# Optimization experiments

Measured on AMD Instinct MI355X. Metric: run time of the kernel, lower is better.

Reference implementation:

```python
import jax, jax.numpy as jnp
import numpy as np

B, C, H, W = 16, 256, 64, 64

def setup_inputs() -> dict:
    key = jax.random.key(0)
    ks = jax.random.split(key, 4)
    scale = 1.0 / np.sqrt(C)
    return {
        "x": jax.random.normal(ks[0], (B, C, H, W), dtype=jnp.float32),
        "w1": jax.random.normal(ks[1], (C, C), dtype=jnp.float32) * scale,
        "b1": jnp.zeros((C,), dtype=jnp.float32),
        "w2": jax.random.normal(ks[2], (C, C), dtype=jnp.float32) * scale,
        "b2": jnp.zeros((C,), dtype=jnp.float32),
        "w3": jax.random.normal(ks[3], (C, C), dtype=jnp.float32) * scale,
        "b3": jnp.zeros((C,), dtype=jnp.float32),
    }

def reference(x, w1, b1, w2, b2, w3, b3):
    b, c, h, w = x.shape
    n = h * w
    # 1x1 convs == per-pixel linear maps over channels; w has shape [C_out, C_in]
    def proj(wt, bias):
        return jnp.einsum('bchw,oc->bohw', x, wt) + bias[None, :, None, None]
    v = proj(w1, b1).reshape(b, c, n).transpose(0, 2, 1)   # [B, N, C]
    q = proj(w2, b2).reshape(b, c, n)                      # [B, C, N]
    k = proj(w3, b3).reshape(b, c, n)                      # [B, C, N]
    weight = jnp.einsum('bcn,bdn->bcd', q, k)              # [B, C, C]
    # global softmax over the entire flattened C*C matrix per batch element
    weight = jax.nn.softmax(weight.reshape(b, -1), axis=1).reshape(b, c, c)
    out = jnp.einsum('bnc,bcd->bdn', v, weight)            # [B, C, N]
    return out.reshape(x.shape)
```

## Files before the change

### kernel.cpp

```cpp
#include <hip/hip_runtime.h>


typedef unsigned short u16;
typedef __attribute__((ext_vector_type(8))) short short8;
typedef __attribute__((ext_vector_type(4))) float floatx4;

__device__ __forceinline__ u16 f2b(float f) {
  union { float f; unsigned int u; } v; v.f = f;
  unsigned int u = v.u;
  return (u16)((u + 0x7fffu + ((u >> 16) & 1u)) >> 16);
}
__device__ __forceinline__ float b2f(u16 h) {
  union { unsigned int u; float f; } v; v.u = ((unsigned int)h) << 16;
  return v.f;
}

__global__ __launch_bounds__(256) void prep_w_kernel(
    const float* __restrict__ w1, const float* __restrict__ w2, const float* __restrict__ w3,
    u16* __restrict__ W1Th, u16* __restrict__ W2h, u16* __restrict__ W2l,
    u16* __restrict__ W3h, u16* __restrict__ W3l, float* __restrict__ xsum) {
  const int blk = blockIdx.x, t = threadIdx.x;
  if (blk == 576) {
#pragma unroll
    for (int i = 0; i < 16; ++i) xsum[t + i * 256] = 0.f;
    return;
  }
  if (blk < 64) {
    __shared__ float tile[32][33];
    const int e0 = (blk & 7) * 32, c0 = (blk >> 3) * 32;
    const int tx = t & 31, ty = t >> 5;
#pragma unroll
    for (int i = 0; i < 4; ++i)
      tile[ty + i * 8][tx] = w1[(c0 + ty + i * 8) * 256 + e0 + tx];
    __syncthreads();
#pragma unroll
    for (int i = 0; i < 4; ++i)
      W1Th[(e0 + ty + i * 8) * 256 + c0 + tx] = f2b(tile[tx][ty + i * 8]);
  } else {
    const int i = (blk - 64) * 256 + t;
    const int e = i & 0xffff;
    const float f = (i >> 16) ? w3[e] : w2[e];
    u16 h = f2b(f);
    if (i >> 16) { W3h[e] = h; W3l[e] = f2b(f - b2f(h)); }
    else         { W2h[e] = h; W2l[e] = f2b(f - b2f(h)); }
  }
}

__device__ __forceinline__ void stage8(const float4 a, const float4 b,
                                       u16* dH, u16* dL, float& xa) {
  const float f[8] = {a.x, a.y, a.z, a.w, b.x, b.y, b.z, b.w};
  union { u16 h8[8]; uint4 q; } uh, ul;
#pragma unroll
  for (int i = 0; i < 8; ++i) {
    const u16 hi = f2b(f[i]);
    uh.h8[i] = hi;
    ul.h8[i] = f2b(f[i] - b2f(hi));
    xa += f[i];
  }
  *(uint4*)dH = uh.q;
  *(uint4*)dL = ul.q;
}

__global__ __launch_bounds__(512, 2) void gram_kernel(
    const float* __restrict__ x, float* __restrict__ Gp, float* __restrict__ xsum) {
  constexpr int LR = 40;
  __shared__ u16 lH[2][256 * LR], lL[2][256 * LR];
  const int b = blockIdx.x >> 4, s = (blockIdx.x >> 1) & 7, mh = blockIdx.x & 1;
  const float* Xb = x + (long)b * 1048576 + s * 512;
  const int t = threadIdx.x;
  const int lane = t & 63, wave = t >> 6;
  const int quad = lane >> 4, l16 = lane & 15;
  const int wml = (wave & 1) * 64 + mh * 128;
  const int wn = (wave >> 1) * 64;
  const int r0 = t >> 2, qc = (t & 3) * 8;
  const int r1 = r0 + 128;
  floatx4 acc[4][4] = {};
  float xa0 = 0.f, xa1 = 0.f;
  float4 p[4];
  p[0] = *(const float4*)(Xb + (long)r0 * 4096 + qc);
  p[1] = *(const float4*)(Xb + (long)r0 * 4096 + qc + 4);
  p[2] = *(const float4*)(Xb + (long)r1 * 4096 + qc);
  p[3] = *(const float4*)(Xb + (long)r1 * 4096 + qc + 4);
  stage8(p[0], p[1], lH[0] + r0 * LR + qc, lL[0] + r0 * LR + qc, xa0);
  stage8(p[2], p[3], lH[0] + r1 * LR + qc, lL[0] + r1 * LR + qc, xa1);
  __syncthreads();
  for (int kb = 0; kb < 16; ++kb) {
    const int cur = kb & 1, nxt = cur ^ 1;
    if (kb < 15) {
      const long kk = (kb + 1) * 32;
      p[0] = *(const float4*)(Xb + (long)r0 * 4096 + kk + qc);
      p[1] = *(const float4*)(Xb + (long)r0 * 4096 + kk + qc + 4);
      p[2] = *(const float4*)(Xb + (long)r1 * 4096 + kk + qc);
      p[3] = *(const float4*)(Xb + (long)r1 * 4096 + kk + qc + 4);
    }
    const u16* cH = lH[cur];
    const u16* cL = lL[cur];
    short8 ah[4], al[4];
#pragma unroll
    for (int i = 0; i < 4; ++i) {
      ah[i] = *(const short8*)(cH + (wml + i * 16 + l16) * LR + quad * 8);
      al[i] = *(const short8*)(cL + (wml + i * 16 + l16) * LR + quad * 8);
    }
#pragma unroll
    for (int j = 0; j < 4; ++j) {
      const short8 bh = *(const short8*)(cH + (wn + j * 16 + l16) * LR + quad * 8);
      const short8 bl = *(const short8*)(cL + (wn + j * 16 + l16) * LR + quad * 8);
#pragma unroll
      for (int i = 0; i < 4; ++i) {
        acc[i][j] = __builtin_amdgcn_mfma_f32_16x16x32_bf16(ah[i], bh, acc[i][j], 0, 0, 0);
        acc[i][j] = __builtin_amdgcn_mfma_f32_16x16x32_bf16(ah[i], bl, acc[i][j], 0, 0, 0);
        acc[i][j] = __builtin_amdgcn_mfma_f32_16x16x32_bf16(al[i], bh, acc[i][j], 0, 0, 0);
      }
    }
    if (kb < 15) {
      stage8(p[0], p[1], lH[nxt] + r0 * LR + qc, lL[nxt] + r0 * LR + qc, xa0);
      stage8(p[2], p[3], lH[nxt] + r1 * LR + qc, lL[nxt] + r1 * LR + qc, xa1);
    }
    __syncthreads();
  }
  if (mh == 0) {
    float v = xa0;
    v += __shfl_xor(v, 1);
    v += __shfl_xor(v, 2);
    if ((t & 3) == 0) atomicAdd(&xsum[b * 256 + r0], v);
    v = xa1;
    v += __shfl_xor(v, 1);
    v += __shfl_xor(v, 2);
    if ((t & 3) == 0) atomicAdd(&xsum[b * 256 + r1], v);
  }
  float* G = Gp + ((long)b * 8 + s) * 65536;
#pragma unroll
  for (int i = 0; i < 4; ++i) {
    const int row0 = wml + i * 16 + quad * 4;
#pragma unroll
    for (int j = 0; j < 4; ++j) {
      const int col = wn + j * 16 + l16;
#pragma unroll
      for (int r = 0; r < 4; ++r)
        G[(long)(row0 + r) * 256 + col] = acc[i][j][r];
    }
  }
}

__global__ void reduce_g_kernel(const float* __restrict__ Gp, u16* __restrict__ Gh,
                                u16* __restrict__ Gl) {
  const long e = (long)blockIdx.x * 256 + threadIdx.x;
  const long base = ((e >> 16) << 19) + (e & 65535);
  float s = 0.f;
#pragma unroll
  for (int i = 0; i < 8; ++i) s += Gp[base + (long)i * 65536];
  u16 h = f2b(s);
  Gh[e] = h;
  Gl[e] = f2b(s - b2f(h));
}

template <bool X3, int EPI>
__global__ __launch_bounds__(256) void gemm_small(
    const u16* __restrict__ Ah, const u16* __restrict__ Al,
    const u16* __restrict__ Bh, const u16* __restrict__ Bl,
    long aBatch, long bBatch, long oBatch,
    float* __restrict__ outF, u16* __restrict__ outH, u16* __restrict__ outL) {
  constexpr int LR = 40;
  __shared__ u16 smem[(X3 ? 4 : 2) * 64 * LR];
  u16* lAh = smem;
  u16* lBh = smem + 64 * LR;
  u16* lAl = X3 ? (smem + 2 * 64 * LR) : nullptr;
  u16* lBl = X3 ? (smem + 3 * 64 * LR) : nullptr;
  const int b = blockIdx.z;
  const int tm = blockIdx.x & 3, tn = blockIdx.x >> 2;
  const u16* Ahb = Ah + (long)b * aBatch + (long)tm * 64 * 256;
  const u16* Bhb = Bh + (long)b * bBatch + (long)tn * 64 * 256;
  const u16* Alb = X3 ? (Al + (long)b * aBatch + (long)tm * 64 * 256) : nullptr;
  const u16* Blb = X3 ? (Bl + (long)b * bBatch + (long)tn * 64 * 256) : nullptr;
  const int t = threadIdx.x;
  const int lane = t & 63, wave = t >> 6;
  const int quad = lane >> 4, l16 = lane & 15;
  const int wm = (wave & 1) * 32, wn = (wave >> 1) * 32;
  const int r = t >> 2, qc = (t & 3) * 8;
  floatx4 acc[2][2] = {};
  for (int kk = 0; kk < 256; kk += 32) {
    __syncthreads();
    *(uint4*)(lAh + r * LR + qc) = *(const uint4*)(Ahb + (long)r * 256 + kk + qc);
    *(uint4*)(lBh + r * LR + qc) = *(const uint4*)(Bhb + (long)r * 256 + kk + qc);
    if (X3) {
      *(uint4*)(lAl + r * LR + qc) = *(const uint4*)(Alb + (long)r * 256 + kk + qc);
      *(uint4*)(lBl + r * LR + qc) = *(const uint4*)(Blb + (long)r * 256 + kk + qc);
    }
    __syncthreads();
    short8 afh[2], bfh[2], afl[2], bfl[2];
#pragma unroll
    for (int i = 0; i < 2; ++i) {
      afh[i] = *(const short8*)(lAh + (wm + i * 16 + l16) * LR + quad * 8);
      bfh[i] = *(const short8*)(lBh + (wn + i * 16 + l16) * LR + quad * 8);
      if (X3) {
        afl[i] = *(const short8*)(lAl + (wm + i * 16 + l16) * LR + quad * 8);
        bfl[i] = *(const short8*)(lBl + (wn + i * 16 + l16) * LR + quad * 8);
      }
    }
#pragma unroll
    for (int i = 0; i < 2; ++i)
#pragma unroll
      for (int j = 0; j < 2; ++j) {
        acc[i][j] = __builtin_amdgcn_mfma_f32_16x16x32_bf16(afh[i], bfh[j], acc[i][j], 0, 0, 0);
        if (X3) {
          acc[i][j] = __builtin_amdgcn_mfma_f32_16x16x32_bf16(afh[i], bfl[j], acc[i][j], 0, 0, 0);
          acc[i][j] = __builtin_amdgcn_mfma_f32_16x16x32_bf16(afl[i], bfh[j], acc[i][j], 0, 0, 0);
        }
      }
  }
  const long obase = (long)b * oBatch;
#pragma unroll
  for (int i = 0; i < 2; ++i) {
    const int mb = tm * 64 + wm + i * 16 + quad * 4;
#pragma unroll
    for (int j = 0; j < 2; ++j) {
      const int n = tn * 64 + wn + j * 16 + l16;
#pragma unroll
      for (int rr = 0; rr < 4; ++rr) {
        const float v = acc[i][j][rr];
        const long idx = obase + (long)(mb + rr) * 256 + n;
        if (EPI == 0) {
          outF[idx] = v;
        } else if (EPI == 1) {
          u16 h = f2b(v);
          outH[idx] = h;
          outL[idx] = f2b(v - b2f(h));
        } else {
          outH[idx] = f2b(v);
        }
      }
    }
  }
}

__global__ __launch_bounds__(256, 2) void gemm_out(
    const u16* __restrict__ Mh, const float* __restrict__ x,
    const float* __restrict__ bb, float* __restrict__ out) {
  constexpr int LR = 40;
  __shared__ u16 lA[256 * LR], lB[128 * LR];
  const int b = blockIdx.z;
  const int tn = blockIdx.x;
  const u16* Ab = Mh + (long)b * 65536;
  const float* Xb = x + (long)b * 1048576 + tn * 128;
  const int t = threadIdx.x;
  const int lane = t & 63, wave = t >> 6;
  const int quad = lane >> 4, l16 = lane & 15;
  const int wm = wave * 64;
  const int erp = (t >> 4) * 2;
  const int n0 = (t & 15) * 8;
  floatx4 acc[4][8] = {};
  for (int kk = 0; kk < 256; kk += 32) {
    __syncthreads();
#pragma unroll
    for (int h = 0; h < 4; ++h) {
      const int r = (t >> 2) + h * 64;
      *(uint4*)(lA + r * LR + (t & 3) * 8) =
          *(const uint4*)(Ab + (long)r * 256 + kk + (t & 3) * 8);
    }
    {
      const float4 a0 = *(const float4*)(Xb + (long)(kk + erp) * 4096 + n0);
      const float4 a1 = *(const float4*)(Xb + (long)(kk + erp) * 4096 + n0 + 4);
      const float4 c0 = *(const float4*)(Xb + (long)(kk + erp + 1) * 4096 + n0);
      const float4 c1 = *(const float4*)(Xb + (long)(kk + erp + 1) * 4096 + n0 + 4);
      const float fa[8] = {a0.x, a0.y, a0.z, a0.w, a1.x, a1.y, a1.z, a1.w};
      const float fc[8] = {c0.x, c0.y, c0.z, c0.w, c1.x, c1.y, c1.z, c1.w};
#pragma unroll
      for (int i = 0; i < 8; ++i) {
        const int nl = n0 + i;
        const int sb = (erp >> 3) ^ ((nl >> 4) & 3);
        const unsigned int pk =
            (unsigned int)f2b(fa[i]) | ((unsigned int)f2b(fc[i]) << 16);
        *(unsigned int*)(lB + nl * LR + sb * 8 + (erp & 7)) = pk;
      }
    }
    __syncthreads();
    short8 af[4], bf[8];
#pragma unroll
    for (int j = 0; j < 8; ++j) {
      const int n = j * 16 + l16;
      const int rb = quad ^ ((n >> 4) & 3);
      bf[j] = *(const short8*)(lB + n * LR + rb * 8);
    }
#pragma unroll
    for (int i = 0; i < 4; ++i)
      af[i] = *(const short8*)(lA + (wm + i * 16 + l16) * LR + quad * 8);
#pragma unroll
    for (int i = 0; i < 4; ++i)
#pragma unroll
      for (int j = 0; j < 8; ++j)
        acc[i][j] = __builtin_amdgcn_mfma_f32_16x16x32_bf16(af[i], bf[j], acc[i][j], 0, 0, 0);
  }
  const long obase = (long)b * 1048576;
#pragma unroll
  for (int i = 0; i < 4; ++i) {
    const int mb = wm + i * 16 + quad * 4;
#pragma unroll
    for (int j = 0; j < 8; ++j) {
      const int n = tn * 128 + j * 16 + l16;
#pragma unroll
      for (int r = 0; r < 4; ++r)
        out[obase + (long)(mb + r) * 4096 + n] = acc[i][j][r] + bb[b * 256 + mb + r];
    }
  }
}

__global__ __launch_bounds__(512) void bias_prep_kernel(
    const float* __restrict__ w2, const float* __restrict__ w3,
    const float* __restrict__ xsum, float* __restrict__ S2, float* __restrict__ S3) {
  __shared__ float xs[256];
  const int b = blockIdx.x, t = threadIdx.x;
  if (t < 256) xs[t] = xsum[b * 256 + t];
  __syncthreads();
  const float* wm = (t < 256) ? w2 : w3;
  const int a = t & 255;
  float s = 0.f;
#pragma unroll 4
  for (int c = 0; c < 256; ++c) s += wm[a * 256 + c] * xs[c];
  if (t < 256) S2[b * 256 + a] = s;
  else         S3[b * 256 + a] = s;
}

__global__ __launch_bounds__(256) void softmax_pass1(
    const float* __restrict__ Lt, const float* __restrict__ S2, const float* __restrict__ S3,
    const float* __restrict__ b2, const float* __restrict__ b3,
    float* __restrict__ bm, float* __restrict__ bs) {
  __shared__ float ls2[256], lb2[256];
  __shared__ float redm[4], reds[4];
  const int b = blockIdx.y, blk = blockIdx.x, t = threadIdx.x;
  ls2[t] = S2[b * 256 + t];
  lb2[t] = b2[t];
  __syncthreads();
  const int fw0 = blk * 2048 + t * 8;
  const int d = fw0 >> 8, a0 = fw0 & 255;
  const float c1 = b3[d];
  const float c0 = S3[b * 256 + d] + 4096.f * c1;
  const long base = (long)b * 65536 + fw0;
  float4 v0 = *(const float4*)(Lt + base);
  float4 v1 = *(const float4*)(Lt + base + 4);
  float v[8] = {v0.x, v0.y, v0.z, v0.w, v1.x, v1.y, v1.z, v1.w};
  float m = -3.4e38f;
#pragma unroll
  for (int i = 0; i < 8; ++i) {
    v[i] += lb2[a0 + i] * c0 + c1 * ls2[a0 + i];
    m = fmaxf(m, v[i]);
  }
  for (int o = 32; o; o >>= 1) m = fmaxf(m, __shfl_xor(m, o));
  const int wid = t >> 6, lane = t & 63;
  if (lane == 0) redm[wid] = m;
  __syncthreads();
  const float bmax = fmaxf(fmaxf(redm[0], redm[1]), fmaxf(redm[2], redm[3]));
  float s = 0.f;
#pragma unroll
  for (int i = 0; i < 8; ++i) s += __expf(v[i] - bmax);
  for (int o = 32; o; o >>= 1) s += __shfl_xor(s, o);
  if (lane == 0) reds[wid] = s;
  __syncthreads();
  if (t == 0) {
    bm[b * 32 + blk] = bmax;
    bs[b * 32 + blk] = reds[0] + reds[1] + reds[2] + reds[3];
  }
}

__global__ __launch_bounds__(256) void softmax_pass3(
    const float* __restrict__ Lt, const float* __restrict__ S2, const float* __restrict__ S3,
    const float* __restrict__ b2, const float* __restrict__ b3,
    const float* __restrict__ bm, const float* __restrict__ bs,
    const float* __restrict__ b1, u16* __restrict__ WTh, float* __restrict__ bb) {
  __shared__ float ls2[256], lb2[256], lb1[256];
  __shared__ float sM, sInv;
  const int b = blockIdx.y, blk = blockIdx.x, t = threadIdx.x;
  if (t < 64) {
    const float m = (t < 32) ? bm[b * 32 + t] : -3.4e38f;
    float s = (t < 32) ? bs[b * 32 + t] : 0.f;
    float M = m;
    for (int o = 32; o; o >>= 1) M = fmaxf(M, __shfl_xor(M, o));
    s *= __expf(m - M);
    for (int o = 32; o; o >>= 1) s += __shfl_xor(s, o);
    if (t == 0) { sM = M; sInv = 1.0f / s; }
  }
  ls2[t] = S2[b * 256 + t];
  lb2[t] = b2[t];
  lb1[t] = b1[t];
  __syncthreads();
  const float M = sM, inv = sInv;
  const int fw0 = blk * 2048 + t * 8;
  const int d = fw0 >> 8, a0 = fw0 & 255;
  const float c1 = b3[d];
  const float c0 = S3[b * 256 + d] + 4096.f * c1;
  const long base = (long)b * 65536 + fw0;
  float4 v0 = *(const float4*)(Lt + base);
  float4 v1 = *(const float4*)(Lt + base + 4);
  float v[8] = {v0.x, v0.y, v0.z, v0.w, v1.x, v1.y, v1.z, v1.w};
  union { u16 h[8]; uint4 q; } o;
  float bsum = 0.f;
#pragma unroll
  for (int i = 0; i < 8; ++i) {
    const float vv = v[i] + lb2[a0 + i] * c0 + c1 * ls2[a0 + i];
    const float w = __expf(vv - M) * inv;
    o.h[i] = f2b(w);
    bsum += w * lb1[a0 + i];
  }
  *(uint4*)(WTh + base) = o.q;
  for (int off = 16; off; off >>= 1) bsum += __shfl_xor(bsum, off);
  if ((t & 31) == 0) bb[b * 256 + d] = bsum;
}

extern "C" void kernel_launch(void* const* d_in, const int* in_sizes, int n_in,
                              void* d_out, int out_size, void* d_ws, size_t ws_size,
                              hipStream_t stream) {
  const float* x  = (const float*)d_in[0];
  const float* w1 = (const float*)d_in[1];
  const float* b1 = (const float*)d_in[2];
  const float* w2 = (const float*)d_in[3];
  const float* b2 = (const float*)d_in[4];
  const float* w3 = (const float*)d_in[5];
  const float* b3 = (const float*)d_in[6];
  float* out = (float*)d_out;

  char* ws = (char*)d_ws;
  size_t off = 0;
  auto alloc = [&](size_t bytes) {
    void* p = ws + off;
    off += (bytes + 255) & ~(size_t)255;
    return p;
  };
  float* Gp = (float*)alloc(8ull * 16 * 65536 * 4);
  float* xsum = (float*)alloc(16 * 256 * 4);
  u16* Gh   = (u16*)alloc(16ull * 65536 * 2);
  u16* Gl   = (u16*)alloc(16ull * 65536 * 2);
  u16* T3h  = (u16*)alloc(16ull * 65536 * 2);
  u16* T3l  = (u16*)alloc(16ull * 65536 * 2);
  float* Lb = (float*)alloc(16ull * 65536 * 4);
  u16* WTh  = (u16*)alloc(16ull * 65536 * 2);
  u16* Mh   = (u16*)alloc(16ull * 65536 * 2);
  u16* W1Th = (u16*)alloc(65536 * 2);
  u16* W2h  = (u16*)alloc(65536 * 2);
  u16* W2l  = (u16*)alloc(65536 * 2);
  u16* W3h  = (u16*)alloc(65536 * 2);
  u16* W3l  = (u16*)alloc(65536 * 2);
  float* S2   = (float*)alloc(16 * 256 * 4);
  float* S3   = (float*)alloc(16 * 256 * 4);
  float* bmx  = (float*)alloc(16 * 32 * 4);
  float* bsx  = (float*)alloc(16 * 32 * 4);
  float* bb   = (float*)alloc(16 * 256 * 4);

  prep_w_kernel<<<577, 256, 0, stream>>>(w1, w2, w3, W1Th, W2h, W2l, W3h, W3l, xsum);

  gram_kernel<<<256, 512, 0, stream>>>(x, Gp, xsum);
  reduce_g_kernel<<<4096, 256, 0, stream>>>(Gp, Gh, Gl);

  gemm_small<true, 1><<<dim3(16, 1, 16), 256, 0, stream>>>(
      W3h, W3l, Gh, Gl, 0, 65536, 65536, nullptr, T3h, T3l);
  gemm_small<true, 0><<<dim3(16, 1, 16), 256, 0, stream>>>(
      T3h, T3l, W2h, W2l, 65536, 0, 65536, Lb, nullptr, nullptr);

  bias_prep_kernel<<<16, 512, 0, stream>>>(w2, w3, xsum, S2, S3);
  softmax_pass1<<<dim3(32, 16), 256, 0, stream>>>(Lb, S2, S3, b2, b3, bmx, bsx);
  softmax_pass3<<<dim3(32, 16), 256, 0, stream>>>(Lb, S2, S3, b2, b3, bmx, bsx,
                                                  b1, WTh, bb);

  gemm_small<false, 2><<<dim3(16, 1, 16), 256, 0, stream>>>(
      WTh, nullptr, W1Th, nullptr, 65536, 0, 65536, nullptr, Mh, nullptr);
  gemm_out<<<dim3(32, 1, 16), 256, 0, stream>>>(Mh, x, bb, out);
}
```

Measured before the change: 217.4 us.

## Split gram over more K-slices, swizzle LDS, packed bf16 cvt, register-prefetch GEMMs

The gram kernel now splits the pixel dimension into 16 slices instead of 8, doubling the grid to 512 blocks. Its LDS tiles drop the padding in favour of an XOR swizzle, and the launch bound asks for 4 blocks per CU. Float-to-bf16 conversion uses the packed v_cvt_pk_bf16_f32 instruction in place of manual rounding. gemm_small and gemm_out gain register prefetch of the next K tile so global loads overlap the MFMA work. In exchange, the partial Gram buffer doubles, which means more write traffic and a heavier reduce_g pass.

```diff
diff --git a/kernel.cpp b/kernel.cpp
--- a/kernel.cpp
+++ b/kernel.cpp
@@ -13,6 +13,11 @@
 __device__ __forceinline__ float b2f(u16 h) {
   union { unsigned int u; float f; } v; v.u = ((unsigned int)h) << 16;
   return v.f;
+}
+__device__ __forceinline__ unsigned int cvt_pk_bf16(float lo, float hi) {
+  unsigned int r;
+  asm("v_cvt_pk_bf16_f32 %0, %1, %2" : "=v"(r) : "v"(lo), "v"(hi));
+  return r;
 }
 
 __global__ __launch_bounds__(256) void prep_w_kernel(
@@ -49,24 +54,26 @@
 __device__ __forceinline__ void stage8(const float4 a, const float4 b,
                                        u16* dH, u16* dL, float& xa) {
   const float f[8] = {a.x, a.y, a.z, a.w, b.x, b.y, b.z, b.w};
-  union { u16 h8[8]; uint4 q; } uh, ul;
-#pragma unroll
-  for (int i = 0; i < 8; ++i) {
-    const u16 hi = f2b(f[i]);
-    uh.h8[i] = hi;
-    ul.h8[i] = f2b(f[i] - b2f(hi));
-    xa += f[i];
+  union { unsigned int w[4]; uint4 q; } uh, ul;
+#pragma unroll
+  for (int i = 0; i < 4; ++i) {
+    const unsigned int h = cvt_pk_bf16(f[2 * i], f[2 * i + 1]);
+    uh.w[i] = h;
+    union { unsigned int u; float ff; } h0, h1;
+    h0.u = h << 16;
+    h1.u = h & 0xffff0000u;
+    ul.w[i] = cvt_pk_bf16(f[2 * i] - h0.ff, f[2 * i + 1] - h1.ff);
+    xa += f[2 * i] + f[2 * i + 1];
   }
   *(uint4*)dH = uh.q;
   *(uint4*)dL = ul.q;
 }
 
-__global__ __launch_bounds__(512, 2) void gram_kernel(
+__global__ __launch_bounds__(512, 4) void gram_kernel(
     const float* __restrict__ x, float* __restrict__ Gp, float* __restrict__ xsum) {
-  constexpr int LR = 40;
-  __shared__ u16 lH[2][256 * LR], lL[2][256 * LR];
-  const int b = blockIdx.x >> 4, s = (blockIdx.x >> 1) & 7, mh = blockIdx.x & 1;
-  const float* Xb = x + (long)b * 1048576 + s * 512;
+  __shared__ u16 lH[2][256 * 32], lL[2][256 * 32];
+  const int b = blockIdx.x >> 5, s = (blockIdx.x >> 1) & 15, mh = blockIdx.x & 1;
+  const float* Xb = x + (long)b * 1048576 + s * 256;
   const int t = threadIdx.x;
   const int lane = t & 63, wave = t >> 6;
   const int quad = lane >> 4, l16 = lane & 15;
@@ -74,6 +81,8 @@
   const int wn = (wave >> 1) * 64;
   const int r0 = t >> 2, qc = (t & 3) * 8;
   const int r1 = r0 + 128;
+  const int wq = (((t & 3) ^ ((r0 >> 1) & 3))) * 8;
+  const int rq = ((quad ^ ((l16 >> 1) & 3))) * 8;
   floatx4 acc[4][4] = {};
   float xa0 = 0.f, xa1 = 0.f;
   float4 p[4];
@@ -81,12 +90,12 @@
   p[1] = *(const float4*)(Xb + (long)r0 * 4096 + qc + 4);
   p[2] = *(const float4*)(Xb + (long)r1 * 4096 + qc);
   p[3] = *(const float4*)(Xb + (long)r1 * 4096 + qc + 4);
-  stage8(p[0], p[1], lH[0] + r0 * LR + qc, lL[0] + r0 * LR + qc, xa0);
-  stage8(p[2], p[3], lH[0] + r1 * LR + qc, lL[0] + r1 * LR + qc, xa1);
+  stage8(p[0], p[1], lH[0] + r0 * 32 + wq, lL[0] + r0 * 32 + wq, xa0);
+  stage8(p[2], p[3], lH[0] + r1 * 32 + wq, lL[0] + r1 * 32 + wq, xa1);
   __syncthreads();
-  for (int kb = 0; kb < 16; ++kb) {
+  for (int kb = 0; kb < 8; ++kb) {
     const int cur = kb & 1, nxt = cur ^ 1;
-    if (kb < 15) {
+    if (kb < 7) {
       const long kk = (kb + 1) * 32;
       p[0] = *(const float4*)(Xb + (long)r0 * 4096 + kk + qc);
       p[1] = *(const float4*)(Xb + (long)r0 * 4096 + kk + qc + 4);
@@ -98,13 +107,13 @@
     short8 ah[4], al[4];
 #pragma unroll
     for (int i = 0; i < 4; ++i) {
-      ah[i] = *(const short8*)(cH + (wml + i * 16 + l16) * LR + quad * 8);
-      al[i] = *(const short8*)(cL + (wml + i * 16 + l16) * LR + quad * 8);
+      ah[i] = *(const short8*)(cH + (wml + i * 16 + l16) * 32 + rq);
+      al[i] = *(const short8*)(cL + (wml + i * 16 + l16) * 32 + rq);
     }
 #pragma unroll
     for (int j = 0; j < 4; ++j) {
-      const short8 bh = *(const short8*)(cH + (wn + j * 16 + l16) * LR + quad * 8);
-      const short8 bl = *(const short8*)(cL + (wn + j * 16 + l16) * LR + quad * 8);
+      const short8 bh = *(const short8*)(cH + (wn + j * 16 + l16) * 32 + rq);
+      const short8 bl = *(const short8*)(cL + (wn + j * 16 + l16) * 32 + rq);
 #pragma unroll
       for (int i = 0; i < 4; ++i) {
         acc[i][j] = __builtin_amdgcn_mfma_f32_16x16x32_bf16(ah[i], bh, acc[i][j], 0, 0, 0);
@@ -112,9 +121,9 @@
         acc[i][j] = __builtin_amdgcn_mfma_f32_16x16x32_bf16(al[i], bh, acc[i][j], 0, 0, 0);
       }
     }
-    if (kb < 15) {
-      stage8(p[0], p[1], lH[nxt] + r0 * LR + qc, lL[nxt] + r0 * LR + qc, xa0);
-      stage8(p[2], p[3], lH[nxt] + r1 * LR + qc, lL[nxt] + r1 * LR + qc, xa1);
+    if (kb < 7) {
+      stage8(p[0], p[1], lH[nxt] + r0 * 32 + wq, lL[nxt] + r0 * 32 + wq, xa0);
+      stage8(p[2], p[3], lH[nxt] + r1 * 32 + wq, lL[nxt] + r1 * 32 + wq, xa1);
     }
     __syncthreads();
   }
@@ -128,7 +137,7 @@
     v += __shfl_xor(v, 2);
     if ((t & 3) == 0) atomicAdd(&xsum[b * 256 + r1], v);
   }
-  float* G = Gp + ((long)b * 8 + s) * 65536;
+  float* G = Gp + ((long)b * 16 + s) * 65536;
 #pragma unroll
   for (int i = 0; i < 4; ++i) {
     const int row0 = wml + i * 16 + quad * 4;
@@ -145,10 +154,10 @@
 __global__ void reduce_g_kernel(const float* __restrict__ Gp, u16* __restrict__ Gh,
                                 u16* __restrict__ Gl) {
   const long e = (long)blockIdx.x * 256 + threadIdx.x;
-  const long base = ((e >> 16) << 19) + (e & 65535);
+  const long base = ((e >> 16) << 20) + (e & 65535);
   float s = 0.f;
 #pragma unroll
-  for (int i = 0; i < 8; ++i) s += Gp[base + (long)i * 65536];
+  for (int i = 0; i < 16; ++i) s += Gp[base + (long)i * 65536];
   u16 h = f2b(s);
   Gh[e] = h;
   Gl[e] = f2b(s - b2f(h));
@@ -178,15 +187,30 @@
   const int wm = (wave & 1) * 32, wn = (wave >> 1) * 32;
   const int r = t >> 2, qc = (t & 3) * 8;
   floatx4 acc[2][2] = {};
+  uint4 pA, pB, pAl = {}, pBl = {};
+  pA = *(const uint4*)(Ahb + (long)r * 256 + qc);
+  pB = *(const uint4*)(Bhb + (long)r * 256 + qc);
+  if (X3) {
+    pAl = *(const uint4*)(Alb + (long)r * 256 + qc);
+    pBl = *(const uint4*)(Blb + (long)r * 256 + qc);
+  }
   for (int kk = 0; kk < 256; kk += 32) {
     __syncthreads();
-    *(uint4*)(lAh + r * LR + qc) = *(const uint4*)(Ahb + (long)r * 256 + kk + qc);
-    *(uint4*)(lBh + r * LR + qc) = *(const uint4*)(Bhb + (long)r * 256 + kk + qc);
+    *(uint4*)(lAh + r * LR + qc) = pA;
+    *(uint4*)(lBh + r * LR + qc) = pB;
     if (X3) {
-      *(uint4*)(lAl + r * LR + qc) = *(const uint4*)(Alb + (long)r * 256 + kk + qc);
-      *(uint4*)(lBl + r * LR + qc) = *(const uint4*)(Blb + (long)r * 256 + kk + qc);
+      *(uint4*)(lAl + r * LR + qc) = pAl;
+      *(uint4*)(lBl + r * LR + qc) = pBl;
     }
     __syncthreads();
+    if (kk < 224) {
+      pA = *(const uint4*)(Ahb + (long)r * 256 + kk + 32 + qc);
+      pB = *(const uint4*)(Bhb + (long)r * 256 + kk + 32 + qc);
+      if (X3) {
+        pAl = *(const uint4*)(Alb + (long)r * 256 + kk + 32 + qc);
+        pBl = *(const uint4*)(Blb + (long)r * 256 + kk + 32 + qc);
+      }
+    }
     short8 afh[2], bfh[2], afl[2], bfl[2];
 #pragma unroll
     for (int i = 0; i < 2; ++i) {
@@ -249,31 +273,44 @@
   const int erp = (t >> 4) * 2;
   const int n0 = (t & 15) * 8;
   floatx4 acc[4][8] = {};
+  uint4 pA[4];
+  float4 pb0, pb1, pb2, pb3;
+#pragma unroll
+  for (int h = 0; h < 4; ++h)
+    pA[h] = *(const uint4*)(Ab + (long)((t >> 2) + h * 64) * 256 + (t & 3) * 8);
+  pb0 = *(const float4*)(Xb + (long)erp * 4096 + n0);
+  pb1 = *(const float4*)(Xb + (long)erp * 4096 + n0 + 4);
+  pb2 = *(const float4*)(Xb + (long)(erp + 1) * 4096 + n0);
+  pb3 = *(const float4*)(Xb + (long)(erp + 1) * 4096 + n0 + 4);
   for (int kk = 0; kk < 256; kk += 32) {
     __syncthreads();
 #pragma unroll
     for (int h = 0; h < 4; ++h) {
       const int r = (t >> 2) + h * 64;
-      *(uint4*)(lA + r * LR + (t & 3) * 8) =
-          *(const uint4*)(Ab + (long)r * 256 + kk + (t & 3) * 8);
+      *(uint4*)(lA + r * LR + (t & 3) * 8) = pA[h];
     }
     {
-      const float4 a0 = *(const float4*)(Xb + (long)(kk + erp) * 4096 + n0);
-      const float4 a1 = *(const float4*)(Xb + (long)(kk + erp) * 4096 + n0 + 4);
-      const float4 c0 = *(const float4*)(Xb + (long)(kk + erp + 1) * 4096 + n0);
-      const float4 c1 = *(const float4*)(Xb + (long)(kk + erp + 1) * 4096 + n0 + 4);
-      const float fa[8] = {a0.x, a0.y, a0.z, a0.w, a1.x, a1.y, a1.z, a1.w};
-      const float fc[8] = {c0.x, c0.y, c0.z, c0.w, c1.x, c1.y, c1.z, c1.w};
+      const float fa[8] = {pb0.x, pb0.y, pb0.z, pb0.w, pb1.x, pb1.y, pb1.z, pb1.w};
+      const float fc[8] = {pb2.x, pb2.y, pb2.z, pb2.w, pb3.x, pb3.y, pb3.z, pb3.w};
 #pragma unroll
       for (int i = 0; i < 8; ++i) {
         const int nl = n0 + i;
         const int sb = (erp >> 3) ^ ((nl >> 4) & 3);
-        const unsigned int pk =
-            (unsigned int)f2b(fa[i]) | ((unsigned int)f2b(fc[i]) << 16);
-        *(unsigned int*)(lB + nl * LR + sb * 8 + (erp & 7)) = pk;
+        *(unsigned int*)(lB + nl * LR + sb * 8 + (erp & 7)) =
+            cvt_pk_bf16(fa[i], fc[i]);
       }
     }
     __syncthreads();
+    if (kk < 224) {
+      const int k2 = kk + 32;
+#pragma unroll
+      for (int h = 0; h < 4; ++h)
+        pA[h] = *(const uint4*)(Ab + (long)((t >> 2) + h * 64) * 256 + k2 + (t & 3) * 8);
+      pb0 = *(const float4*)(Xb + (long)(k2 + erp) * 4096 + n0);
+      pb1 = *(const float4*)(Xb + (long)(k2 + erp) * 4096 + n0 + 4);
+      pb2 = *(const float4*)(Xb + (long)(k2 + erp + 1) * 4096 + n0);
+      pb3 = *(const float4*)(Xb + (long)(k2 + erp + 1) * 4096 + n0 + 4);
+    }
     short8 af[4], bf[8];
 #pragma unroll
     for (int j = 0; j < 8; ++j) {
@@ -424,7 +461,7 @@
     off += (bytes + 255) & ~(size_t)255;
     return p;
   };
-  float* Gp = (float*)alloc(8ull * 16 * 65536 * 4);
+  float* Gp = (float*)alloc(16ull * 16 * 65536 * 4);
   float* xsum = (float*)alloc(16 * 256 * 4);
   u16* Gh   = (u16*)alloc(16ull * 65536 * 2);
   u16* Gl   = (u16*)alloc(16ull * 65536 * 2);
@@ -446,7 +483,7 @@
 
   prep_w_kernel<<<577, 256, 0, stream>>>(w1, w2, w3, W1Th, W2h, W2l, W3h, W3l, xsum);
 
-  gram_kernel<<<256, 512, 0, stream>>>(x, Gp, xsum);
+  gram_kernel<<<512, 512, 0, stream>>>(x, Gp, xsum);
   reduce_g_kernel<<<4096, 256, 0, stream>>>(Gp, Gh, Gl);
 
   gemm_small<true, 1><<<dim3(16, 1, 16), 256, 0, stream>>>(
```

Result: slower. 233.9 us (+7.6%).
